# Optimization experiments

Measured on AMD Instinct MI355X. Metric: run time of the kernel, lower is better.

Reference implementation:

```python
import jax, jax.numpy as jnp
import numpy as np

# MambaLayer_image(channels=48, scan_modes=[0,1,2], d_state=8) on [B,C,D,H,W]
C = 48          # channels (d_model of BidirectionalMambaBlocks)
DM = C // 2     # d_model per direction-mamba = 24
DIN = 2 * DM    # mamba d_inner (expand=2) = 48
DS = 8          # d_state
DC = 4          # d_conv
DTR = max(1, -(-DM // 16))  # dt_rank = ceil(24/16) = 2
B, D, H, W = 2, 32, 32, 32


def setup_inputs():
    key = jax.random.key(0)
    ks = jax.random.split(key, 8)
    s = 0.05
    A_init = jnp.tile(jnp.arange(1, DS + 1, dtype=jnp.float32), (6, DIN, 1))
    return {
        "x": jax.random.normal(ks[0], (B, C, D, H, W), jnp.float32),
        "ln_g": jnp.ones((3, C), jnp.float32),
        "ln_b": jnp.zeros((3, C), jnp.float32),
        "in_w": jax.random.normal(ks[1], (6, 2 * DIN, DM), jnp.float32) * s,
        "conv_w": jax.random.normal(ks[2], (6, DIN, DC), jnp.float32) * s,
        "conv_b": jnp.zeros((6, DIN), jnp.float32),
        "xproj_w": jax.random.normal(ks[3], (6, DTR + 2 * DS, DIN), jnp.float32) * s,
        "dt_w": jax.random.normal(ks[4], (6, DIN, DTR), jnp.float32) * s,
        "dt_b": jax.random.normal(ks[5], (6, DIN), jnp.float32) * 0.1,
        "A_log": jnp.log(A_init),
        "Dp": jnp.ones((6, DIN), jnp.float32),
        "out_w": jax.random.normal(ks[6], (6, DM, DIN), jnp.float32) * s,
    }


def _layernorm(x, g, b, eps=1e-5):
    mu = jnp.mean(x, axis=-1, keepdims=True)
    var = jnp.mean(jnp.square(x - mu), axis=-1, keepdims=True)
    return (x - mu) * jax.lax.rsqrt(var + eps) * g + b


def _mamba(u, p):
    """Standard mamba_ssm Mamba forward. u: [B, L, DM] -> [B, L, DM]."""
    in_w, cw, cb, xw, dtw, dtb, Alog, Dpar, ow = p
    xz = jnp.einsum('bld,ed->ble', u, in_w)          # [B,L,2*DIN]
    xc, z = jnp.split(xz, 2, axis=-1)
    L = xc.shape[1]
    # causal depthwise conv1d over L (kernel DC)
    xpad = jnp.pad(xc, ((0, 0), (DC - 1, 0), (0, 0)))
    xc = sum(xpad[:, k:k + L, :] * cw[:, k] for k in range(DC)) + cb
    xc = jax.nn.silu(xc)
    xdbl = jnp.einsum('bld,ed->ble', xc, xw)          # [B,L,DTR+2*DS]
    dt_in = xdbl[..., :DTR]
    Bm = xdbl[..., DTR:DTR + DS]
    Cm = xdbl[..., DTR + DS:]
    dt = jax.nn.softplus(jnp.einsum('blr,dr->bld', dt_in, dtw) + dtb)  # [B,L,DIN]
    A = -jnp.exp(Alog)                                # [DIN,DS]
    dA = jnp.exp(dt[..., None] * A)                   # [B,L,DIN,DS]
    dBx = dt[..., None] * Bm[:, :, None, :] * xc[..., None]

    def step(h, inp):
        dA_t, dBx_t, C_t = inp
        h = dA_t * h + dBx_t                          # [B,DIN,DS]
        return h, jnp.einsum('bds,bs->bd', h, C_t)

    h0 = jnp.zeros((xc.shape[0], DIN, DS), xc.dtype)
    _, ys = jax.lax.scan(step, h0, (jnp.swapaxes(dA, 0, 1),
                                    jnp.swapaxes(dBx, 0, 1),
                                    jnp.swapaxes(Cm, 0, 1)))
    y = jnp.swapaxes(ys, 0, 1) + xc * Dpar            # [B,L,DIN]
    y = y * jax.nn.silu(z)
    return jnp.einsum('bld,ed->ble', y, ow)           # [B,L,DM]


def _bimamba(xflat, g, b, pf, pb):
    res = xflat
    xn = _layernorm(xflat, g, b)
    xf, xb = jnp.split(xn, 2, axis=-1)
    of = _mamba(xf, pf)
    ob = jnp.flip(_mamba(jnp.flip(xb, axis=1), pb), axis=1)
    return jnp.concatenate([of, ob], axis=-1) + res


def _forward(x, ln_g, ln_b, in_w, conv_w, conv_b, xproj_w, dt_w, dt_b, A_log, Dp, out_w):
    Bn, Cn = x.shape[0], x.shape[1]
    perms = [None, (0, 1, 3, 4, 2), (0, 1, 4, 2, 3)]   # DHW, HWD, WDH
    invs = [None, (0, 1, 4, 2, 3), (0, 1, 3, 4, 2)]
    packs = (in_w, conv_w, conv_b, xproj_w, dt_w, dt_b, A_log, Dp, out_w)
    cur = x
    for i in range(3):
        xp = cur if perms[i] is None else jnp.transpose(cur, perms[i])
        shp = xp.shape
        xf = jnp.swapaxes(xp.reshape(Bn, Cn, -1), 1, 2)   # [B,L,C]
        pf = tuple(a[2 * i] for a in packs)
        pb = tuple(a[2 * i + 1] for a in packs)
        xm = _bimamba(xf, ln_g[i], ln_b[i], pf, pb)
        xo = jnp.swapaxes(xm, 1, 2).reshape(shp)
        cur = xo if invs[i] is None else jnp.transpose(xo, invs[i])
    return cur + x


def reference(x, ln_g, ln_b, in_w, conv_w, conv_b, xproj_w, dt_w, dt_b, A_log, Dp, out_w):
    return _forward(x, ln_g, ln_b, in_w, conv_w, conv_b, xproj_w, dt_w, dt_b, A_log, Dp, out_w)
```

## Files before the change

### kernel.cpp

```cpp
#include <hip/hip_runtime.h>
#include <math.h>

#define LL   32768
#define NCH  1024
#define LC   32
#define BL48 3145728
#define ROW48(g,l) (((size_t)(g)*LL + (l))*48)
#define ROW16(g,l) (((size_t)(g)*LL + (l))*16)

typedef unsigned short ushort_t;
typedef ushort_t ushort8 __attribute__((ext_vector_type(8)));

__device__ __forceinline__ float sigmoidf_(float x){ return 1.0f/(1.0f+__expf(-x)); }
__device__ __forceinline__ float softplusf_(float x){ return (x > 20.0f) ? x : log1pf(__expf(x)); }
__device__ __forceinline__ ushort_t f2bf(float f){
  union { float f; unsigned u; } v; v.f = f;
  unsigned r = v.u + 0x7FFFu + ((v.u >> 16) & 1u);
  return (ushort_t)(r >> 16);
}
__device__ __forceinline__ float bf2f(ushort_t h){
  union { unsigned u; float f; } v; v.u = ((unsigned)h) << 16;
  return v.f;
}

extern "C" __global__ void __launch_bounds__(64)
k_flat(const float* __restrict__ cur,
       const float* __restrict__ lng, const float* __restrict__ lnb,
       const float* __restrict__ in_w, const float* __restrict__ conv_w,
       const float* __restrict__ conv_b, const float* __restrict__ xproj_w,
       const float* __restrict__ dt_w, const float* __restrict__ dt_b,
       ushort_t* __restrict__ dtb, ushort_t* __restrict__ xcb,
       ushort_t* __restrict__ zb, ushort_t* __restrict__ BCB, int orient)
{
  const int lane = threadIdx.x;
  const int wid  = blockIdx.x;
  const int b    = blockIdx.y;
  const int dir  = blockIdx.z;
  const int j    = 2*orient + dir;
  const int g    = 2*dir + b;
  const int ch0  = dir*24;
  const int l    = wid*61 - 3 + lane;
  const bool inr = (l >= 0 && l < LL);
  const bool own = inr && (dir ? (lane <= 60) : (lane >= 3));

  float u[24];
  if (inr){
    const float* p = cur + (size_t)b*48*LL + l;
    float v[48]; float mu = 0.f;
    #pragma unroll
    for (int c2 = 0; c2 < 48; c2++){ v[c2] = p[(size_t)c2*LL]; mu += v[c2]; }
    mu *= (1.f/48.f);
    float var = 0.f;
    #pragma unroll
    for (int c2 = 0; c2 < 48; c2++){ float dd = v[c2]-mu; var += dd*dd; }
    float rstd = rsqrtf(var*(1.f/48.f) + 1e-5f);
    #pragma unroll
    for (int c2 = 0; c2 < 24; c2++)
      u[c2] = (v[ch0+c2]-mu)*rstd*lng[ch0+c2] + lnb[ch0+c2];
  } else {
    #pragma unroll
    for (int c2 = 0; c2 < 24; c2++) u[c2] = 0.f;
  }

  const float* iw = in_w + j*2304;
  const float* cw = conv_w + j*192;
  const float* cb = conv_b + j*48;
  const float* xw = xproj_w + j*864;
  const int pos = dir ? (LL-1-l) : l;
  ushort_t* xcr = xcb + ROW48(g, pos);

  float xd[18];
  #pragma unroll
  for (int q = 0; q < 18; q++) xd[q] = 0.f;
  #pragma unroll
  for (int d0 = 0; d0 < 48; d0 += 8){
    ushort8 oxc;
    #pragma unroll
    for (int k = 0; k < 8; k++){
      const int d = d0 + k;
      float xzv = 0.f;
      #pragma unroll
      for (int c2 = 0; c2 < 24; c2++) xzv += u[c2]*iw[d*24+c2];
      float t1, t2, t3;
      if (dir){ t1 = __shfl_down(xzv,1); t2 = __shfl_down(xzv,2); t3 = __shfl_down(xzv,3); }
      else    { t1 = __shfl_up(xzv,1);   t2 = __shfl_up(xzv,2);   t3 = __shfl_up(xzv,3); }
      float acc = cb[d] + cw[d*4+3]*xzv + cw[d*4+2]*t1 + cw[d*4+1]*t2 + cw[d*4+0]*t3;
      acc = acc * sigmoidf_(acc);
      oxc[k] = f2bf(acc);
      #pragma unroll
      for (int q = 0; q < 18; q++) xd[q] += acc*xw[q*48+d];
    }
    if (own) *(ushort8*)(xcr + d0) = oxc;
  }

  const float* dw = dt_w + j*96;
  const float* db = dt_b + j*48;
  ushort_t* dtr = dtb + ROW48(g, pos);
  #pragma unroll
  for (int d0 = 0; d0 < 48; d0 += 8){
    ushort8 o;
    #pragma unroll
    for (int k = 0; k < 8; k++){
      const int d = d0 + k;
      o[k] = f2bf(softplusf_(xd[0]*dw[d*2] + xd[1]*dw[d*2+1] + db[d]));
    }
    if (own) *(ushort8*)(dtr + d0) = o;
  }

  if (own){
    ushort_t* bc = BCB + ROW16(g, pos);
    ushort8 ob, oc;
    #pragma unroll
    for (int k = 0; k < 8; k++){ ob[k] = f2bf(xd[2+k]); oc[k] = f2bf(xd[10+k]); }
    *(ushort8*)(bc)   = ob;
    *(ushort8*)(bc+8) = oc;
  }

  ushort_t* zr = zb + ROW48(g, pos);
  #pragma unroll
  for (int e0 = 48; e0 < 96; e0 += 8){
    ushort8 o;
    #pragma unroll
    for (int k = 0; k < 8; k++){
      float s = 0.f;
      #pragma unroll
      for (int c2 = 0; c2 < 24; c2++) s += u[c2]*iw[(e0+k)*24+c2];
      o[k] = f2bf(s);
    }
    if (own) *(ushort8*)(zr + (e0-48)) = o;
  }
}

extern "C" __global__ void __launch_bounds__(192)
k_scan1(const ushort_t* __restrict__ dtb, const ushort_t* __restrict__ xcb,
        const ushort_t* __restrict__ BCB, const float* __restrict__ A_log,
        float* __restrict__ PS, int orient)
{
  const int d = threadIdx.x % 48;
  const int sid = blockIdx.x*4 + threadIdx.x/48;
  const int c = sid & (NCH-1);
  const int g = sid >> 10;
  const int dir = g >> 1;
  const float* Al = A_log + (2*orient+dir)*384 + d*8;
  float A[8], P[8], S[8];
  #pragma unroll
  for (int s = 0; s < 8; s++){ A[s] = -__expf(Al[s]); P[s]=1.f; S[s]=0.f; }
  const ushort_t* pdt = dtb + ROW48(g, c*LC) + d;
  const ushort_t* pxc = xcb + ROW48(g, c*LC) + d;
  const ushort_t* pbc = BCB + ROW16(g, c*LC);
  #pragma unroll 4
  for (int j = 0; j < LC; j++){
    float dtv = bf2f(pdt[(size_t)j*48]);
    float xcv = bf2f(pxc[(size_t)j*48]);
    ushort8 br = *(const ushort8*)(pbc + (size_t)j*16);
    float dx = dtv*xcv;
    #pragma unroll
    for (int s = 0; s < 8; s++){
      float dA = __expf(dtv*A[s]);
      P[s] *= dA;
      S[s] = S[s]*dA + dx*bf2f(br[s]);
    }
  }
  float* out = PS + ((size_t)g*NCH + c)*768 + d*8;
  *(float4*)(out)       = make_float4(P[0],P[1],P[2],P[3]);
  *(float4*)(out+4)     = make_float4(P[4],P[5],P[6],P[7]);
  *(float4*)(out+384)   = make_float4(S[0],S[1],S[2],S[3]);
  *(float4*)(out+388)   = make_float4(S[4],S[5],S[6],S[7]);
}

extern "C" __global__ void __launch_bounds__(256)
k_scan2(float* __restrict__ PS)
{
  const int t = blockIdx.x*256 + threadIdx.x;
  const int chain = t >> 6;
  const int lane  = t & 63;
  const int g  = chain / 384;
  const int st = chain % 384;
  float* base = PS + (size_t)g*NCH*768 + st;
  float P[16], S[16];
  const int c0 = lane*16;
  #pragma unroll
  for (int k = 0; k < 16; k++){
    P[k] = base[(size_t)(c0+k)*768];
    S[k] = base[(size_t)(c0+k)*768 + 384];
  }
  float Pl = 1.f, Sl = 0.f;
  #pragma unroll
  for (int k = 0; k < 16; k++){ Sl = P[k]*Sl + S[k]; Pl = P[k]*Pl; }
  float Pi = Pl, Si = Sl;
  #pragma unroll
  for (int off = 1; off < 64; off <<= 1){
    float Pp = __shfl_up(Pi, off);
    float Sp = __shfl_up(Si, off);
    if (lane >= off){ Si = Pi*Sp + Si; Pi = Pi*Pp; }
  }
  float h = __shfl_up(Si, 1);
  if (lane == 0) h = 0.f;
  #pragma unroll
  for (int k = 0; k < 16; k++){
    base[(size_t)(c0+k)*768 + 384] = h;
    h = fmaf(P[k], h, S[k]);
  }
}

extern "C" __global__ void __launch_bounds__(192)
k_scan3c(const ushort_t* __restrict__ dtb, const ushort_t* __restrict__ xcb,
         const ushort_t* __restrict__ zb, const ushort_t* __restrict__ BCB,
         const float* __restrict__ A_log, const float* __restrict__ Dp,
         const float* __restrict__ PS, const float* __restrict__ out_w,
         const float* __restrict__ resid, float* __restrict__ outp, int orient)
{
  __shared__ ushort_t yt[4][32][50];
  const int t = threadIdx.x;
  const int d  = t % 48;
  const int pr = t / 48;
  const int b  = blockIdx.y;
  const int dir = blockIdx.z;
  const int bx = blockIdx.x;
  const int g = 2*dir + b;
  const int j = 2*orient + dir;
  const int cf = bx*4 + pr;
  const int c  = dir ? (NCH-1-cf) : cf;

  {
    const float* Al = A_log + j*384 + d*8;
    const float* hp = PS + ((size_t)g*NCH + c)*768 + 384 + d*8;
    float A[8], h[8];
    float4 h0 = *(const float4*)(hp);
    float4 h1 = *(const float4*)(hp+4);
    h[0]=h0.x; h[1]=h0.y; h[2]=h0.z; h[3]=h0.w;
    h[4]=h1.x; h[5]=h1.y; h[6]=h1.z; h[7]=h1.w;
    #pragma unroll
    for (int s = 0; s < 8; s++) A[s] = -__expf(Al[s]);
    const float Dpd = Dp[j*48 + d];
    const ushort_t* pdt = dtb + ROW48(g, c*LC) + d;
    const ushort_t* pxc = xcb + ROW48(g, c*LC) + d;
    const ushort_t* pz  = zb  + ROW48(g, c*LC) + d;
    const ushort_t* pbc = BCB + ROW16(g, c*LC);
    for (int j2 = 0; j2 < LC; j2++){
      float dtv = bf2f(pdt[(size_t)j2*48]);
      float xcv = bf2f(pxc[(size_t)j2*48]);
      float zv  = bf2f(pz [(size_t)j2*48]);
      ushort8 br = *(const ushort8*)(pbc + (size_t)j2*16);
      ushort8 cr = *(const ushort8*)(pbc + (size_t)j2*16 + 8);
      float dx = dtv*xcv;
      float y = 0.f;
      #pragma unroll
      for (int s = 0; s < 8; s++){
        float dA = __expf(dtv*A[s]);
        h[s] = h[s]*dA + dx*bf2f(br[s]);
        y += h[s]*bf2f(cr[s]);
      }
      y += xcv*Dpd;
      int sl = dir ? (31-j2) : j2;
      yt[pr][sl][d] = f2bf(y * (zv * sigmoidf_(zv)));
    }
  }
  __syncthreads();

  if (t < 128){
    const int sub = t >> 5, pp = t & 31;
    const int l = bx*128 + sub*32 + pp;
    const float* ow = out_w + (size_t)j*1152;
    float o[24];
    #pragma unroll
    for (int e = 0; e < 24; e++) o[e]=0.f;
    for (int dd = 0; dd < 48; dd++){
      float vv = bf2f(yt[sub][pp][dd]);
      #pragma unroll
      for (int e = 0; e < 24; e++) o[e] += vv*ow[e*48+dd];
    }
    const size_t pb = (size_t)b*48*LL + (size_t)(dir*24)*LL + l;
    #pragma unroll
    for (int e = 0; e < 24; e++){
      outp[pb + (size_t)e*LL] = o[e] + resid[pb + (size_t)e*LL];
    }
  }
}

extern "C" __global__ void __launch_bounds__(256)
k_perm(const float* __restrict__ in, const float* __restrict__ xadd,
       float* __restrict__ out, int addx)
{
  __shared__ float t[32][33];
  const int q = blockIdx.y;
  const float* ip = in + (size_t)q*LL;
  float* op = out + (size_t)q*LL;
  const int ab0 = blockIdx.x*32;
  const int tx = threadIdx.x & 31, ty = threadIdx.x >> 5;
  #pragma unroll
  for (int k = 0; k < 4; k++){
    int c = ty + 8*k;
    t[c][tx] = ip[(size_t)c*1024 + ab0 + tx];
  }
  __syncthreads();
  #pragma unroll
  for (int k = 0; k < 4; k++){
    int ab = ty + 8*k;
    float v = t[tx][ab];
    size_t o = (size_t)(ab0+ab)*32 + tx;
    if (addx) v += xadd[(size_t)q*LL + o];
    op[o] = v;
  }
}

extern "C" void kernel_launch(void* const* d_in, const int* in_sizes, int n_in,
                              void* d_out, int out_size, void* d_ws, size_t ws_size,
                              hipStream_t stream)
{
  const float* x       = (const float*)d_in[0];
  const float* ln_g    = (const float*)d_in[1];
  const float* ln_b    = (const float*)d_in[2];
  const float* in_w    = (const float*)d_in[3];
  const float* conv_w  = (const float*)d_in[4];
  const float* conv_b  = (const float*)d_in[5];
  const float* xproj_w = (const float*)d_in[6];
  const float* dt_w    = (const float*)d_in[7];
  const float* dt_b    = (const float*)d_in[8];
  const float* A_log   = (const float*)d_in[9];
  const float* Dp      = (const float*)d_in[10];
  const float* out_w   = (const float*)d_in[11];
  float* out = (float*)d_out;

  char* w = (char*)d_ws;
  ushort_t* dtb  = (ushort_t*)w;  w += (size_t)4*LL*48*2;
  ushort_t* xcb  = (ushort_t*)w;  w += (size_t)4*LL*48*2;
  ushort_t* zbuf = (ushort_t*)w;  w += (size_t)4*LL*48*2;
  ushort_t* BCB  = (ushort_t*)w;  w += (size_t)4*LL*16*2;
  float*    PS   = (float*)w;     w += (size_t)4*NCH*768*4;
  float*    sout = (float*)w;     w += (size_t)BL48*4;
  float*    curT = (float*)w;     w += (size_t)BL48*4;

  for (int i = 0; i < 3; i++){
    const float* ip;
    if (i == 0) ip = x;
    else {
      k_perm<<<dim3(32, 96), 256, 0, stream>>>(sout, x, curT, 0);
      ip = curT;
    }
    k_flat<<<dim3(540, 2, 2), 64, 0, stream>>>(ip, ln_g + i*48, ln_b + i*48,
        in_w, conv_w, conv_b, xproj_w, dt_w, dt_b, dtb, xcb, zbuf, BCB, i);
    k_scan1<<<dim3(NCH), 192, 0, stream>>>(dtb, xcb, BCB, A_log, PS, i);
    k_scan2<<<dim3(384), 256, 0, stream>>>(PS);
    k_scan3c<<<dim3(NCH/4, 2, 2), 192, 0, stream>>>(dtb, xcb, zbuf, BCB,
        A_log, Dp, PS, out_w, ip, sout, i);
  }
  k_perm<<<dim3(32, 96), 256, 0, stream>>>(sout, x, out, 1);
}
```

Measured before the change: 588.7 us.

## Store inter-stage activations in bf16 and split k_flat channels across waves

The input and intermediate activations (residual stream, permuted buffers, scan outputs) are now kept in bf16 instead of fp32, with a new conversion kernel at the start. This halves memory traffic for the layernorm reads, residual reads and transposes. k_flat now runs 256-thread blocks where two waves split the 48 inner channels and combine their partial x_proj sums through shared memory, which adds parallelism per position. The layernorm switches to a one-pass sum/sum-of-squares variance. Rounding the residual stream to bf16 at every stage adds precision error that compounds across the three orientations.

```diff
diff --git a/kernel.cpp b/kernel.cpp
--- a/kernel.cpp
+++ b/kernel.cpp
@@ -10,6 +10,7 @@
 
 typedef unsigned short ushort_t;
 typedef ushort_t ushort8 __attribute__((ext_vector_type(8)));
+typedef ushort_t ushort4v __attribute__((ext_vector_type(4)));
 
 __device__ __forceinline__ float sigmoidf_(float x){ return 1.0f/(1.0f+__expf(-x)); }
 __device__ __forceinline__ float softplusf_(float x){ return (x > 20.0f) ? x : log1pf(__expf(x)); }
@@ -23,8 +24,17 @@
   return v.f;
 }
 
-extern "C" __global__ void __launch_bounds__(64)
-k_flat(const float* __restrict__ cur,
+extern "C" __global__ void __launch_bounds__(256)
+k_tobf(const float* __restrict__ in, ushort_t* __restrict__ out)
+{
+  const size_t i = ((size_t)blockIdx.x*256 + threadIdx.x)*4;
+  float4 v = *(const float4*)(in + i);
+  ushort4v o; o[0]=f2bf(v.x); o[1]=f2bf(v.y); o[2]=f2bf(v.z); o[3]=f2bf(v.w);
+  *(ushort4v*)(out + i) = o;
+}
+
+extern "C" __global__ void __launch_bounds__(256, 4)
+k_flat(const ushort_t* __restrict__ curb,
        const float* __restrict__ lng, const float* __restrict__ lnb,
        const float* __restrict__ in_w, const float* __restrict__ conv_w,
        const float* __restrict__ conv_b, const float* __restrict__ xproj_w,
@@ -32,31 +42,44 @@
        ushort_t* __restrict__ dtb, ushort_t* __restrict__ xcb,
        ushort_t* __restrict__ zb, ushort_t* __restrict__ BCB, int orient)
 {
-  const int lane = threadIdx.x;
-  const int wid  = blockIdx.x;
+  __shared__ float sx[2][2][64][10];
+  const int tid  = threadIdx.x;
+  const int lane = tid & 63;
+  const int wv   = tid >> 6;
+  const int grp  = wv >> 1;
+  const int half = wv & 1;
+  const int d0   = half*24;
+  const int gidx = blockIdx.x*2 + grp;
   const int b    = blockIdx.y;
   const int dir  = blockIdx.z;
   const int j    = 2*orient + dir;
   const int g    = 2*dir + b;
   const int ch0  = dir*24;
-  const int l    = wid*61 - 3 + lane;
+  const int oth  = 24 - ch0;
+  const int l    = gidx*61 - 3 + lane;
   const bool inr = (l >= 0 && l < LL);
   const bool own = inr && (dir ? (lane <= 60) : (lane >= 3));
 
   float u[24];
   if (inr){
-    const float* p = cur + (size_t)b*48*LL + l;
-    float v[48]; float mu = 0.f;
-    #pragma unroll
-    for (int c2 = 0; c2 < 48; c2++){ v[c2] = p[(size_t)c2*LL]; mu += v[c2]; }
-    mu *= (1.f/48.f);
-    float var = 0.f;
-    #pragma unroll
-    for (int c2 = 0; c2 < 48; c2++){ float dd = v[c2]-mu; var += dd*dd; }
-    float rstd = rsqrtf(var*(1.f/48.f) + 1e-5f);
+    const ushort_t* p = curb + (size_t)b*48*LL + l;
+    float sum = 0.f, sq = 0.f;
+    #pragma unroll
+    for (int c2 = 0; c2 < 24; c2++){
+      float vv = bf2f(p[(size_t)(ch0+c2)*LL]);
+      u[c2] = vv; sum += vv; sq += vv*vv;
+    }
+    #pragma unroll
+    for (int c2 = 0; c2 < 24; c2++){
+      float vv = bf2f(p[(size_t)(oth+c2)*LL]);
+      sum += vv; sq += vv*vv;
+    }
+    float mu = sum*(1.f/48.f);
+    float var = sq*(1.f/48.f) - mu*mu;
+    float rstd = rsqrtf(var + 1e-5f);
     #pragma unroll
     for (int c2 = 0; c2 < 24; c2++)
-      u[c2] = (v[ch0+c2]-mu)*rstd*lng[ch0+c2] + lnb[ch0+c2];
+      u[c2] = (u[c2]-mu)*rstd*lng[ch0+c2] + lnb[ch0+c2];
   } else {
     #pragma unroll
     for (int c2 = 0; c2 < 24; c2++) u[c2] = 0.f;
@@ -67,17 +90,17 @@
   const float* cb = conv_b + j*48;
   const float* xw = xproj_w + j*864;
   const int pos = dir ? (LL-1-l) : l;
-  ushort_t* xcr = xcb + ROW48(g, pos);
 
   float xd[18];
   #pragma unroll
   for (int q = 0; q < 18; q++) xd[q] = 0.f;
-  #pragma unroll
-  for (int d0 = 0; d0 < 48; d0 += 8){
+  ushort_t* xcr = xcb + ROW48(g, pos) + d0;
+  #pragma unroll
+  for (int dd0 = 0; dd0 < 24; dd0 += 8){
     ushort8 oxc;
     #pragma unroll
     for (int k = 0; k < 8; k++){
-      const int d = d0 + k;
+      const int d = d0 + dd0 + k;
       float xzv = 0.f;
       #pragma unroll
       for (int c2 = 0; c2 < 24; c2++) xzv += u[c2]*iw[d*24+c2];
@@ -90,44 +113,63 @@
       #pragma unroll
       for (int q = 0; q < 18; q++) xd[q] += acc*xw[q*48+d];
     }
-    if (own) *(ushort8*)(xcr + d0) = oxc;
+    if (own) *(ushort8*)(xcr + dd0) = oxc;
+  }
+
+  if (half == 0){
+    sx[grp][0][lane][0] = xd[0]; sx[grp][0][lane][1] = xd[1];
+    #pragma unroll
+    for (int k = 0; k < 8; k++) sx[grp][0][lane][2+k] = xd[10+k];
+  } else {
+    sx[grp][1][lane][0] = xd[0]; sx[grp][1][lane][1] = xd[1];
+    #pragma unroll
+    for (int k = 0; k < 8; k++) sx[grp][1][lane][2+k] = xd[2+k];
+  }
+  __syncthreads();
+  xd[0] += sx[grp][1-half][lane][0];
+  xd[1] += sx[grp][1-half][lane][1];
+  if (half == 0){
+    #pragma unroll
+    for (int k = 0; k < 8; k++) xd[2+k]  += sx[grp][1][lane][2+k];
+  } else {
+    #pragma unroll
+    for (int k = 0; k < 8; k++) xd[10+k] += sx[grp][0][lane][2+k];
   }
 
   const float* dw = dt_w + j*96;
   const float* db = dt_b + j*48;
-  ushort_t* dtr = dtb + ROW48(g, pos);
-  #pragma unroll
-  for (int d0 = 0; d0 < 48; d0 += 8){
+  ushort_t* dtr = dtb + ROW48(g, pos) + d0;
+  #pragma unroll
+  for (int q8 = 0; q8 < 24; q8 += 8){
     ushort8 o;
     #pragma unroll
     for (int k = 0; k < 8; k++){
-      const int d = d0 + k;
+      const int d = d0 + q8 + k;
       o[k] = f2bf(softplusf_(xd[0]*dw[d*2] + xd[1]*dw[d*2+1] + db[d]));
     }
-    if (own) *(ushort8*)(dtr + d0) = o;
+    if (own) *(ushort8*)(dtr + q8) = o;
   }
 
   if (own){
-    ushort_t* bc = BCB + ROW16(g, pos);
-    ushort8 ob, oc;
-    #pragma unroll
-    for (int k = 0; k < 8; k++){ ob[k] = f2bf(xd[2+k]); oc[k] = f2bf(xd[10+k]); }
-    *(ushort8*)(bc)   = ob;
-    *(ushort8*)(bc+8) = oc;
-  }
-
-  ushort_t* zr = zb + ROW48(g, pos);
-  #pragma unroll
-  for (int e0 = 48; e0 < 96; e0 += 8){
     ushort8 o;
     #pragma unroll
+    for (int k = 0; k < 8; k++) o[k] = f2bf(xd[2 + half*8 + k]);
+    *(ushort8*)(BCB + ROW16(g, pos) + half*8) = o;
+  }
+
+  ushort_t* zr = zb + ROW48(g, pos) + d0;
+  #pragma unroll
+  for (int e0 = 0; e0 < 24; e0 += 8){
+    ushort8 o;
+    #pragma unroll
     for (int k = 0; k < 8; k++){
+      const int e = 48 + d0 + e0 + k;
       float s = 0.f;
       #pragma unroll
-      for (int c2 = 0; c2 < 24; c2++) s += u[c2]*iw[(e0+k)*24+c2];
+      for (int c2 = 0; c2 < 24; c2++) s += u[c2]*iw[e*24+c2];
       o[k] = f2bf(s);
     }
-    if (own) *(ushort8*)(zr + (e0-48)) = o;
+    if (own) *(ushort8*)(zr + e0) = o;
   }
 }
 
@@ -208,7 +250,8 @@
          const ushort_t* __restrict__ zb, const ushort_t* __restrict__ BCB,
          const float* __restrict__ A_log, const float* __restrict__ Dp,
          const float* __restrict__ PS, const float* __restrict__ out_w,
-         const float* __restrict__ resid, float* __restrict__ outp, int orient)
+         const ushort_t* __restrict__ resid, ushort_t* __restrict__ outp,
+         int orient)
 {
   __shared__ ushort_t yt[4][32][50];
   const int t = threadIdx.x;
@@ -273,34 +316,54 @@
     const size_t pb = (size_t)b*48*LL + (size_t)(dir*24)*LL + l;
     #pragma unroll
     for (int e = 0; e < 24; e++){
-      outp[pb + (size_t)e*LL] = o[e] + resid[pb + (size_t)e*LL];
+      outp[pb + (size_t)e*LL] = f2bf(o[e] + bf2f(resid[pb + (size_t)e*LL]));
     }
   }
 }
 
 extern "C" __global__ void __launch_bounds__(256)
-k_perm(const float* __restrict__ in, const float* __restrict__ xadd,
-       float* __restrict__ out, int addx)
+k_perm_bf(const ushort_t* __restrict__ in, ushort_t* __restrict__ out)
 {
   __shared__ float t[32][33];
   const int q = blockIdx.y;
-  const float* ip = in + (size_t)q*LL;
+  const ushort_t* ip = in + (size_t)q*LL;
+  ushort_t* op = out + (size_t)q*LL;
+  const int ab0 = blockIdx.x*32;
+  const int tx = threadIdx.x & 31, ty = threadIdx.x >> 5;
+  #pragma unroll
+  for (int k = 0; k < 4; k++){
+    int c = ty + 8*k;
+    t[c][tx] = bf2f(ip[(size_t)c*1024 + ab0 + tx]);
+  }
+  __syncthreads();
+  #pragma unroll
+  for (int k = 0; k < 4; k++){
+    int ab = ty + 8*k;
+    op[(size_t)(ab0+ab)*32 + tx] = f2bf(t[tx][ab]);
+  }
+}
+
+extern "C" __global__ void __launch_bounds__(256)
+k_perm_fin(const ushort_t* __restrict__ in, const float* __restrict__ xadd,
+           float* __restrict__ out)
+{
+  __shared__ float t[32][33];
+  const int q = blockIdx.y;
+  const ushort_t* ip = in + (size_t)q*LL;
   float* op = out + (size_t)q*LL;
   const int ab0 = blockIdx.x*32;
   const int tx = threadIdx.x & 31, ty = threadIdx.x >> 5;
   #pragma unroll
   for (int k = 0; k < 4; k++){
     int c = ty + 8*k;
-    t[c][tx] = ip[(size_t)c*1024 + ab0 + tx];
+    t[c][tx] = bf2f(ip[(size_t)c*1024 + ab0 + tx]);
   }
   __syncthreads();
   #pragma unroll
   for (int k = 0; k < 4; k++){
     int ab = ty + 8*k;
-    float v = t[tx][ab];
     size_t o = (size_t)(ab0+ab)*32 + tx;
-    if (addx) v += xadd[(size_t)q*LL + o];
-    op[o] = v;
+    op[o] = t[tx][ab] + xadd[(size_t)q*LL + o];
   }
 }
 
@@ -328,22 +391,22 @@
   ushort_t* zbuf = (ushort_t*)w;  w += (size_t)4*LL*48*2;
   ushort_t* BCB  = (ushort_t*)w;  w += (size_t)4*LL*16*2;
   float*    PS   = (float*)w;     w += (size_t)4*NCH*768*4;
-  float*    sout = (float*)w;     w += (size_t)BL48*4;
-  float*    curT = (float*)w;     w += (size_t)BL48*4;
+  ushort_t* xb   = (ushort_t*)w;  w += (size_t)BL48*2;
+  ushort_t* soutb= (ushort_t*)w;  w += (size_t)BL48*2;
+  ushort_t* curTb= (ushort_t*)w;  w += (size_t)BL48*2;
+
+  k_tobf<<<dim3(BL48/1024), 256, 0, stream>>>(x, xb);
 
   for (int i = 0; i < 3; i++){
-    const float* ip;
-    if (i == 0) ip = x;
-    else {
-      k_perm<<<dim3(32, 96), 256, 0, stream>>>(sout, x, curT, 0);
-      ip = curT;
-    }
-    k_flat<<<dim3(540, 2, 2), 64, 0, stream>>>(ip, ln_g + i*48, ln_b + i*48,
+    const ushort_t* ip = (i == 0) ? xb : curTb;
+    k_flat<<<dim3(270, 2, 2), 256, 0, stream>>>(ip, ln_g + i*48, ln_b + i*48,
         in_w, conv_w, conv_b, xproj_w, dt_w, dt_b, dtb, xcb, zbuf, BCB, i);
     k_scan1<<<dim3(NCH), 192, 0, stream>>>(dtb, xcb, BCB, A_log, PS, i);
     k_scan2<<<dim3(384), 256, 0, stream>>>(PS);
     k_scan3c<<<dim3(NCH/4, 2, 2), 192, 0, stream>>>(dtb, xcb, zbuf, BCB,
-        A_log, Dp, PS, out_w, ip, sout, i);
-  }
-  k_perm<<<dim3(32, 96), 256, 0, stream>>>(sout, x, out, 1);
-}
+        A_log, Dp, PS, out_w, ip, soutb, i);
+    if (i < 2)
+      k_perm_bf<<<dim3(32, 96), 256, 0, stream>>>(soutb, curTb);
+  }
+  k_perm_fin<<<dim3(32, 96), 256, 0, stream>>>(soutb, x, out);
+}
```

New measurement: 1.648 ms. 180% more time.
